# Optimization experiments

Hardware: AMD Instinct MI355X
Metric: run time of the kernel (lower is better)

The kernel has to match this reference:

```python
import jax, jax.numpy as jnp
import numpy as np

KE_CONST = 14.3996
NUM_GRAPHS = 48
LONG_RANGE_SCALE = 1.0
SQRT2 = 1.41421356  # literal used in the torch jit script


def setup_inputs() -> dict:
    key = jax.random.key(0)
    ks = jax.random.split(key, 10)
    N, F = 6144, 128
    h0 = jax.random.normal(ks[0], (N, F), dtype=jnp.float32)
    h1 = jax.random.normal(ks[1], (N, F), dtype=jnp.float32)
    pos = jax.random.uniform(ks[2], (N, 3), dtype=jnp.float32) * 10.0  # atoms in a ~10A box
    batch = jnp.sort(jax.random.randint(ks[3], (N,), 0, NUM_GRAPHS))
    # q_proj params: Linear(F,F) + SiLU + Linear(F,1,bias=False), init normal(0,0.2)
    q_W1 = jax.random.normal(ks[4], (F, F), dtype=jnp.float32) * 0.2
    q_b1 = jnp.zeros((F,), dtype=jnp.float32)
    q_W2 = jax.random.normal(ks[5], (F, 1), dtype=jnp.float32) * 0.2
    sigma = jnp.asarray(1.0, dtype=jnp.float32)
    # vdw_proj params: Linear(F,F) + SiLU + Linear(F,2)
    s = 1.0 / np.sqrt(F)
    v_W1 = jax.random.normal(ks[6], (F, F), dtype=jnp.float32) * s
    v_b1 = jnp.zeros((F,), dtype=jnp.float32)
    v_W2 = jax.random.normal(ks[7], (F, 2), dtype=jnp.float32) * s
    v_b2 = jnp.zeros((2,), dtype=jnp.float32)
    return {"h0": h0, "h1": h1, "pos": pos, "q_W1": q_W1, "q_b1": q_b1,
            "q_W2": q_W2, "sigma": sigma, "v_W1": v_W1, "v_b1": v_b1,
            "v_W2": v_W2, "v_b2": v_b2, "batch": batch}


def _forward(h0, pos, q_W1, q_b1, q_W2, sigma, v_W1, v_b1, v_W2, v_b2, batch):
    N = h0.shape[0]
    dt = h0.dtype
    # --- charge head: q = Linear(SiLU(Linear(h0))) , per-graph mean-centered ---
    q = jax.nn.silu(h0 @ q_W1 + q_b1) @ q_W2  # [N,1]
    q_sum = jax.ops.segment_sum(q, batch, num_segments=NUM_GRAPHS)  # [G,1]
    counts = jax.ops.segment_sum(jnp.ones((N, 1), dt), batch, num_segments=NUM_GRAPHS)
    q_mean = q_sum / jnp.clip(counts, 1.0)
    q = q - q_mean[batch]
    # --- vdW head: c6, r_vdw = softplus(Linear(SiLU(Linear(h0)))) ---
    vdw_params = jax.nn.silu(h0 @ v_W1 + v_b1) @ v_W2 + v_b2  # [N,2]
    c6 = jax.nn.softplus(vdw_params[:, 0:1])     # [N,1]
    r_vdw = jax.nn.softplus(vdw_params[:, 1:2])  # [N,1]
    # --- dense pairwise geometry (non-periodic branch: cell is None) ---
    diff = pos[:, None, :] - pos[None, :, :]        # [N,N,3]
    dist_sq = jnp.sum(diff * diff, axis=-1)          # [N,N]
    dist = jnp.sqrt(dist_sq + 1e-8)
    batch_mask = batch[:, None] == batch[None, :]
    diag = jnp.eye(N, dtype=bool)
    mask = (batch_mask & ~diag).astype(dt)           # [N,N]
    # --- erf-shielded direct electrostatics ---
    qq = q @ q.T                                     # [N,N]
    shielding = jax.scipy.special.erf(dist / (SQRT2 * sigma))
    e_elec = 0.5 * KE_CONST * jnp.sum(qq * (1.0 / (dist + 1e-8)) * shielding * mask)
    # --- BJ-damped vdW ---
    c6_ij = jnp.sqrt(c6 @ c6.T)
    rvdw_ij = jnp.sqrt(r_vdw @ r_vdw.T)
    damping = dist_sq ** 3 + rvdw_ij ** 6
    e_vdw = 0.5 * jnp.sum(-(c6_ij / (damping + 1e-8)) * mask)
    return (e_elec + e_vdw) * LONG_RANGE_SCALE


def reference(h0, h1, pos, q_W1, q_b1, q_W2, sigma, v_W1, v_b1, v_W2, v_b2, batch):
    # h1 is accepted by the torch forward signature but unused on this path
    return _forward(h0, pos, q_W1, q_b1, q_W2, sigma, v_W1, v_b1, v_W2, v_b2, batch)
```

## Files before the change

kernel.cpp:

```cpp
#include <hip/hip_runtime.h>
#include <math.h>

#define NUM_GRAPHS 48
#define F 128
#define MB 32
#define R 8
#define NPB (NUM_GRAPHS * R)
#define CHUNK 512

__device__ __forceinline__ float softplus_f(float x) {
    return fmaxf(x, 0.0f) + log1pf(expf(-fabsf(x)));
}
__device__ __forceinline__ float silu_f(float x) {
    return x / (1.0f + expf(-x));
}

__global__ __launch_bounds__(256) void mlp_kernel(
    const float* __restrict__ h0,
    const float* __restrict__ qW1, const float* __restrict__ qb1,
    const float* __restrict__ qW2,
    const float* __restrict__ vW1, const float* __restrict__ vb1,
    const float* __restrict__ vW2, const float* __restrict__ vb2,
    const int* __restrict__ batch, int* __restrict__ seg,
    float* __restrict__ q_raw, float* __restrict__ c6s, float* __restrict__ rv3,
    float* __restrict__ out, int N)
{
    __shared__ float h0s[MB][F];
    __shared__ float red[4][16][3];
    const int tid = threadIdx.x;
    const int a0 = blockIdx.x * MB;

    if (blockIdx.x == 0) {
        if (tid == 0) out[0] = 0.0f;
        for (int i = tid; i < N; i += 256) {
            int b = batch[i];
            int prev = (i == 0) ? -1 : batch[i - 1];
            for (int g = prev + 1; g <= b; ++g) seg[g] = i;
            if (i == N - 1) {
                for (int g = b + 1; g <= NUM_GRAPHS; ++g) seg[g] = N;
            }
        }
    }

    for (int idx = tid; idx < MB * (F / 4); idx += 256) {
        int a = idx >> 5;
        int kq = idx & 31;
        int row = a0 + a;
        float4 v = make_float4(0.f, 0.f, 0.f, 0.f);
        if (row < N) v = ((const float4*)(h0 + (size_t)row * F))[kq];
        ((float4*)&h0s[a][0])[kq] = v;
    }
    __syncthreads();

    const int j  = tid & 127;
    const int g2 = tid >> 7;

    float accq[16], accv[16];
    const float qb = qb1[j], vb = vb1[j];
    #pragma unroll
    for (int a = 0; a < 16; ++a) { accq[a] = qb; accv[a] = vb; }

    const float* __restrict__ qc = qW1 + j;
    const float* __restrict__ vc = vW1 + j;

    float wq[4], wv[4];
    #pragma unroll
    for (int u = 0; u < 4; ++u) {
        wq[u] = qc[(size_t)u * F];
        wv[u] = vc[(size_t)u * F];
    }

    for (int k4 = 0; k4 < F / 4; ++k4) {
        int kn = (k4 < F / 4 - 1) ? (k4 + 1) : k4;
        float nq[4], nv[4];
        #pragma unroll
        for (int u = 0; u < 4; ++u) {
            nq[u] = qc[(size_t)(kn * 4 + u) * F];
            nv[u] = vc[(size_t)(kn * 4 + u) * F];
        }
        #pragma unroll
        for (int a = 0; a < 16; ++a) {
            float4 hv = ((const float4*)&h0s[g2 * 16 + a][0])[k4];
            float tq = accq[a];
            tq = fmaf(hv.x, wq[0], tq);
            tq = fmaf(hv.y, wq[1], tq);
            tq = fmaf(hv.z, wq[2], tq);
            tq = fmaf(hv.w, wq[3], tq);
            accq[a] = tq;
            float tv = accv[a];
            tv = fmaf(hv.x, wv[0], tv);
            tv = fmaf(hv.y, wv[1], tv);
            tv = fmaf(hv.z, wv[2], tv);
            tv = fmaf(hv.w, wv[3], tv);
            accv[a] = tv;
        }
        #pragma unroll
        for (int u = 0; u < 4; ++u) { wq[u] = nq[u]; wv[u] = nv[u]; }
    }

    const float w2q = qW2[j];
    const float w20 = vW2[2 * j];
    const float w21 = vW2[2 * j + 1];
    const int wave = tid >> 6;

    #pragma unroll
    for (int a = 0; a < 16; ++a) {
        float pq = silu_f(accq[a]) * w2q;
        float sv = silu_f(accv[a]);
        float p0 = sv * w20;
        float p1 = sv * w21;
        #pragma unroll
        for (int d = 32; d >= 1; d >>= 1) {
            pq += __shfl_xor(pq, d);
            p0 += __shfl_xor(p0, d);
            p1 += __shfl_xor(p1, d);
        }
        if ((tid & 63) == 0) {
            red[wave][a][0] = pq;
            red[wave][a][1] = p0;
            red[wave][a][2] = p1;
        }
    }
    __syncthreads();

    if (tid < MB) {
        int gg = tid >> 4;
        int al = tid & 15;
        int row = a0 + tid;
        if (row < N) {
            float pq = red[2 * gg][al][0] + red[2 * gg + 1][al][0];
            float p0 = red[2 * gg][al][1] + red[2 * gg + 1][al][1];
            float p1 = red[2 * gg][al][2] + red[2 * gg + 1][al][2];
            q_raw[row] = pq;
            c6s[row] = sqrtf(softplus_f(p0 + vb2[0]));
            float r  = softplus_f(p1 + vb2[1]);
            rv3[row] = r * r * r;
        }
    }
}

__global__ __launch_bounds__(256) void pair_kernel(
    const float* __restrict__ pos,
    const float* __restrict__ q_raw,
    const float* __restrict__ c6s, const float* __restrict__ rv3,
    const int* __restrict__ seg, const float* __restrict__ sigma_p,
    float* __restrict__ out)
{
    __shared__ float xs[CHUNK], ys[CHUNK], zs[CHUNK];
    __shared__ float qs[CHUNK], ss[CHUNK], r3[CHUNK];
    __shared__ float wred[4];

    const int g     = blockIdx.x / R;
    const int slice = blockIdx.x % R;
    const int tid   = threadIdx.x;
    const int wave  = tid >> 6;
    const int lane  = tid & 63;
    const int s0 = seg[g], s1 = seg[g + 1];
    const int n = s1 - s0;
    if (n <= 1) return;

    float acc = 0.0f;
    {
        float ms = 0.f;
        for (int i = s0 + lane; i < s1; i += 64) ms += q_raw[i];
        #pragma unroll
        for (int d = 32; d >= 1; d >>= 1) ms += __shfl_xor(ms, d);
        const float mean = ms / (float)n;
        const float inv_ss = 1.0f / (1.41421356f * sigma_p[0]);
        const int wv = slice * 4 + wave;

        for (int c0 = s0; c0 < s1; c0 += CHUNK) {
            const int cn = min(CHUNK, s1 - c0);
            __syncthreads();
            for (int idx = tid; idx < cn; idx += 256) {
                int a = c0 + idx;
                xs[idx] = pos[3 * a + 0];
                ys[idx] = pos[3 * a + 1];
                zs[idx] = pos[3 * a + 2];
                qs[idx] = (q_raw[a] - mean) * (0.5f * 14.3996f);
                ss[idx] = c6s[a] * 0.5f;
                r3[idx] = rv3[a];
            }
            __syncthreads();

            for (int i = s0 + wv; i < s1; i += 4 * R) {
                float xi = pos[3 * i + 0], yi = pos[3 * i + 1], zi = pos[3 * i + 2];
                float qi = q_raw[i] - mean;
                float si = c6s[i];
                float ri = rv3[i];
                for (int jd = lane; jd < cn; jd += 64) {
                    if (c0 + jd == i) continue;
                    float dx = xi - xs[jd];
                    float dy = yi - ys[jd];
                    float dz = zi - zs[jd];
                    float d2 = fmaf(dx, dx, fmaf(dy, dy, dz * dz));
                    float dist = sqrtf(d2 + 1e-8f);
                    float e1 = qi * qs[jd] * erff(dist * inv_ss) / (dist + 1e-8f);
                    float damp = fmaf(d2 * d2, d2, fmaf(ri, r3[jd], 1e-8f));
                    float e2 = si * ss[jd] / damp;
                    acc += e1 - e2;
                }
            }
        }
    }
    #pragma unroll
    for (int d = 32; d >= 1; d >>= 1) acc += __shfl_xor(acc, d);
    if (lane == 0) wred[wave] = acc;
    __syncthreads();
    if (tid == 0) atomicAdd(out, wred[0] + wred[1] + wred[2] + wred[3]);
}

extern "C" void kernel_launch(void* const* d_in, const int* in_sizes, int n_in,
                              void* d_out, int out_size, void* d_ws, size_t ws_size,
                              hipStream_t stream) {
    const float* h0   = (const float*)d_in[0];
    const float* pos  = (const float*)d_in[2];
    const float* qW1  = (const float*)d_in[3];
    const float* qb1  = (const float*)d_in[4];
    const float* qW2  = (const float*)d_in[5];
    const float* sig  = (const float*)d_in[6];
    const float* vW1  = (const float*)d_in[7];
    const float* vb1  = (const float*)d_in[8];
    const float* vW2  = (const float*)d_in[9];
    const float* vb2  = (const float*)d_in[10];
    const int*  batch = (const int*)d_in[11];
    const int N = in_sizes[0] / F;

    char* ws = (char*)d_ws;
    int*   seg   = (int*)ws;
    float* q_raw = (float*)(ws + 1024);
    float* c6s   = q_raw + N;
    float* rv3   = c6s + N;
    float* out   = (float*)d_out;

    mlp_kernel<<<(N + MB - 1) / MB, 256, 0, stream>>>(
        h0, qW1, qb1, qW2, vW1, vb1, vW2, vb2, batch, seg, q_raw, c6s, rv3, out, N);
    pair_kernel<<<NPB, 256, 0, stream>>>(pos, q_raw, c6s, rv3, seg, sig, out);
}
```

Baseline: 115.0 us.

## Split MLP heads across blocks and stage W1 K-chunks in shared memory

The MLP kernel now launches two blocks per 32-row tile, one per head (charge or vdW), which doubles the block count and halves the per-thread accumulators. Weights and h0 are loaded in K-chunks of 32 into shared memory with register prefetch of the next chunk, replacing the old per-thread strided global weight loads. This targets global-load latency and low occupancy in the MLP stage. The cost is extra syncthreads per chunk and h0 being read twice. The grid uses N/TM without rounding up, so a trailing partial tile would be dropped if N were not a multiple of 32.

```diff
diff --git a/kernel.cpp b/kernel.cpp
--- a/kernel.cpp
+++ b/kernel.cpp
@@ -3,7 +3,9 @@
 
 #define NUM_GRAPHS 48
 #define F 128
-#define MB 32
+#define TM 32
+#define KC 32
+#define NCHUNK (F / KC)
 #define R 8
 #define NPB (NUM_GRAPHS * R)
 #define CHUNK 512
@@ -25,10 +27,14 @@
     float* __restrict__ q_raw, float* __restrict__ c6s, float* __restrict__ rv3,
     float* __restrict__ out, int N)
 {
-    __shared__ float h0s[MB][F];
-    __shared__ float red[4][16][3];
-    const int tid = threadIdx.x;
-    const int a0 = blockIdx.x * MB;
+    __shared__ float ws[KC * F];
+    __shared__ float hs[TM * KC];
+    __shared__ float red[4][16][2];
+
+    const int tid  = threadIdx.x;
+    const int head = blockIdx.x & 1;
+    const int tile = blockIdx.x >> 1;
+    const int a0   = tile * TM;
 
     if (blockIdx.x == 0) {
         if (tid == 0) out[0] = 0.0f;
@@ -42,99 +48,113 @@
         }
     }
 
-    for (int idx = tid; idx < MB * (F / 4); idx += 256) {
-        int a = idx >> 5;
-        int kq = idx & 31;
-        int row = a0 + a;
-        float4 v = make_float4(0.f, 0.f, 0.f, 0.f);
-        if (row < N) v = ((const float4*)(h0 + (size_t)row * F))[kq];
-        ((float4*)&h0s[a][0])[kq] = v;
-    }
-    __syncthreads();
+    const float* __restrict__ W1 = head ? vW1 : qW1;
+    const float* __restrict__ b1 = head ? vb1 : qb1;
+    const float4* __restrict__ W14 = (const float4*)W1;
 
     const int j  = tid & 127;
     const int g2 = tid >> 7;
 
-    float accq[16], accv[16];
-    const float qb = qb1[j], vb = vb1[j];
+    float acc[16];
+    const float bias = b1[j];
     #pragma unroll
-    for (int a = 0; a < 16; ++a) { accq[a] = qb; accv[a] = vb; }
-
-    const float* __restrict__ qc = qW1 + j;
-    const float* __restrict__ vc = vW1 + j;
-
-    float wq[4], wv[4];
-    #pragma unroll
-    for (int u = 0; u < 4; ++u) {
-        wq[u] = qc[(size_t)u * F];
-        wv[u] = vc[(size_t)u * F];
-    }
-
-    for (int k4 = 0; k4 < F / 4; ++k4) {
-        int kn = (k4 < F / 4 - 1) ? (k4 + 1) : k4;
-        float nq[4], nv[4];
-        #pragma unroll
-        for (int u = 0; u < 4; ++u) {
-            nq[u] = qc[(size_t)(kn * 4 + u) * F];
-            nv[u] = vc[(size_t)(kn * 4 + u) * F];
-        }
+    for (int a = 0; a < 16; ++a) acc[a] = bias;
+
+    float4* ws4 = (float4*)ws;
+    float4* hs4 = (float4*)hs;
+
+    float4 wreg[4];
+    float4 hreg;
+    {
+        #pragma unroll
+        for (int u = 0; u < 4; ++u)
+            wreg[u] = W14[u * 256 + tid];
+        int a = tid >> 3, k4 = tid & 7;
+        int row = a0 + a;
+        hreg = make_float4(0.f, 0.f, 0.f, 0.f);
+        if (row < N) hreg = ((const float4*)(h0 + (size_t)row * F))[k4];
+    }
+
+    for (int c = 0; c < NCHUNK; ++c) {
+        __syncthreads();
+        #pragma unroll
+        for (int u = 0; u < 4; ++u) ws4[u * 256 + tid] = wreg[u];
+        hs4[tid] = hreg;
+        __syncthreads();
+
+        if (c + 1 < NCHUNK) {
+            int cn = c + 1;
+            #pragma unroll
+            for (int u = 0; u < 4; ++u)
+                wreg[u] = W14[cn * (KC * F / 4) + u * 256 + tid];
+            int a = tid >> 3, k4 = tid & 7;
+            int row = a0 + a;
+            hreg = make_float4(0.f, 0.f, 0.f, 0.f);
+            if (row < N) hreg = ((const float4*)(h0 + (size_t)row * F))[cn * (KC / 4) + k4];
+        }
+
+        #pragma unroll
+        for (int k4 = 0; k4 < KC / 4; ++k4) {
+            float w0 = ws[(k4 * 4 + 0) * F + j];
+            float w1 = ws[(k4 * 4 + 1) * F + j];
+            float w2 = ws[(k4 * 4 + 2) * F + j];
+            float w3 = ws[(k4 * 4 + 3) * F + j];
+            #pragma unroll
+            for (int a = 0; a < 16; ++a) {
+                float4 hv = hs4[(g2 * 16 + a) * (KC / 4) + k4];
+                float t = acc[a];
+                t = fmaf(hv.x, w0, t);
+                t = fmaf(hv.y, w1, t);
+                t = fmaf(hv.z, w2, t);
+                t = fmaf(hv.w, w3, t);
+                acc[a] = t;
+            }
+        }
+    }
+
+    const int wave = tid >> 6;
+    if (head == 0) {
+        const float w2q = qW2[j];
         #pragma unroll
         for (int a = 0; a < 16; ++a) {
-            float4 hv = ((const float4*)&h0s[g2 * 16 + a][0])[k4];
-            float tq = accq[a];
-            tq = fmaf(hv.x, wq[0], tq);
-            tq = fmaf(hv.y, wq[1], tq);
-            tq = fmaf(hv.z, wq[2], tq);
-            tq = fmaf(hv.w, wq[3], tq);
-            accq[a] = tq;
-            float tv = accv[a];
-            tv = fmaf(hv.x, wv[0], tv);
-            tv = fmaf(hv.y, wv[1], tv);
-            tv = fmaf(hv.z, wv[2], tv);
-            tv = fmaf(hv.w, wv[3], tv);
-            accv[a] = tv;
-        }
-        #pragma unroll
-        for (int u = 0; u < 4; ++u) { wq[u] = nq[u]; wv[u] = nv[u]; }
-    }
-
-    const float w2q = qW2[j];
-    const float w20 = vW2[2 * j];
-    const float w21 = vW2[2 * j + 1];
-    const int wave = tid >> 6;
-
-    #pragma unroll
-    for (int a = 0; a < 16; ++a) {
-        float pq = silu_f(accq[a]) * w2q;
-        float sv = silu_f(accv[a]);
-        float p0 = sv * w20;
-        float p1 = sv * w21;
-        #pragma unroll
-        for (int d = 32; d >= 1; d >>= 1) {
-            pq += __shfl_xor(pq, d);
-            p0 += __shfl_xor(p0, d);
-            p1 += __shfl_xor(p1, d);
-        }
-        if ((tid & 63) == 0) {
-            red[wave][a][0] = pq;
-            red[wave][a][1] = p0;
-            red[wave][a][2] = p1;
-        }
-    }
-    __syncthreads();
-
-    if (tid < MB) {
-        int gg = tid >> 4;
-        int al = tid & 15;
-        int row = a0 + tid;
-        if (row < N) {
-            float pq = red[2 * gg][al][0] + red[2 * gg + 1][al][0];
-            float p0 = red[2 * gg][al][1] + red[2 * gg + 1][al][1];
-            float p1 = red[2 * gg][al][2] + red[2 * gg + 1][al][2];
-            q_raw[row] = pq;
-            c6s[row] = sqrtf(softplus_f(p0 + vb2[0]));
-            float r  = softplus_f(p1 + vb2[1]);
-            rv3[row] = r * r * r;
+            float pq = silu_f(acc[a]) * w2q;
+            #pragma unroll
+            for (int d = 32; d >= 1; d >>= 1) pq += __shfl_xor(pq, d);
+            if ((tid & 63) == 0) red[wave][a][0] = pq;
+        }
+        __syncthreads();
+        if (tid < TM) {
+            int gg = tid >> 4, a = tid & 15;
+            int row = a0 + tid;
+            if (row < N)
+                q_raw[row] = red[2 * gg][a][0] + red[2 * gg + 1][a][0];
+        }
+    } else {
+        const float w20 = vW2[2 * j];
+        const float w21 = vW2[2 * j + 1];
+        #pragma unroll
+        for (int a = 0; a < 16; ++a) {
+            float sv = silu_f(acc[a]);
+            float p0 = sv * w20;
+            float p1 = sv * w21;
+            #pragma unroll
+            for (int d = 32; d >= 1; d >>= 1) {
+                p0 += __shfl_xor(p0, d);
+                p1 += __shfl_xor(p1, d);
+            }
+            if ((tid & 63) == 0) { red[wave][a][0] = p0; red[wave][a][1] = p1; }
+        }
+        __syncthreads();
+        if (tid < TM) {
+            int gg = tid >> 4, a = tid & 15;
+            int row = a0 + tid;
+            if (row < N) {
+                float p0 = red[2 * gg][a][0] + red[2 * gg + 1][a][0];
+                float p1 = red[2 * gg][a][1] + red[2 * gg + 1][a][1];
+                c6s[row] = sqrtf(softplus_f(p0 + vb2[0]));
+                float r  = softplus_f(p1 + vb2[1]);
+                rv3[row] = r * r * r;
+            }
         }
     }
 }
@@ -233,7 +253,7 @@
     float* rv3   = c6s + N;
     float* out   = (float*)d_out;
 
-    mlp_kernel<<<(N + MB - 1) / MB, 256, 0, stream>>>(
+    mlp_kernel<<<(N / TM) * 2, 256, 0, stream>>>(
         h0, qW1, qb1, qW2, vW1, vb1, vW2, vb2, batch, seg, q_raw, c6s, rv3, out, N);
     pair_kernel<<<NPB, 256, 0, stream>>>(pos, q_raw, c6s, rv3, seg, sig, out);
 }
```

Result: slower. 119.0 us (+3.5%).
